# Performance work log

Hardware: AMD Instinct MI355X
Metric: run time of the kernel (lower is better)

Reference implementation:

```python
import jax, jax.numpy as jnp
import numpy as np

N_NODES = 50000
N_EDGES = 800000
D = 64
NEG_SLOPE = 0.2


def setup_inputs() -> dict:
    key = jax.random.key(0)
    ks = jax.random.split(key, 16)
    inp = {
        "t": jnp.zeros((1,), jnp.float32),
        "x": jax.random.normal(ks[0], (N_NODES, D), jnp.float32),
        "edge_index": jax.random.randint(ks[1], (2, N_EDGES), 0, N_NODES, jnp.int64),
    }
    # 3 GATConv layers (64->64, 64->64, 64->64), heads=1
    s = 1.0 / np.sqrt(D)
    for li, k0 in zip((1, 2, 3), (2, 6, 10)):
        inp[f"W{li}"] = jax.random.normal(ks[k0], (D, D), jnp.float32) * s
        inp[f"a_src{li}"] = jax.random.normal(ks[k0 + 1], (D,), jnp.float32) * s
        inp[f"a_dst{li}"] = jax.random.normal(ks[k0 + 2], (D,), jnp.float32) * s
        inp[f"b{li}"] = jnp.zeros((D,), jnp.float32)
    return inp


def _gat_conv(x, src, dst, W, a_src, a_dst, b):
    # h = W x  (PyG: lin(x)), per-edge attention, segment softmax over dst
    n = x.shape[0]
    h = x @ W                                   # [N, D]
    score = jax.nn.leaky_relu(h[src] @ a_src + h[dst] @ a_dst, NEG_SLOPE)  # [E]
    smax = jax.ops.segment_max(score, dst, num_segments=n)                 # [N]
    ex = jnp.exp(score - smax[dst])                                        # [E]
    denom = jax.ops.segment_sum(ex, dst, num_segments=n)                   # [N]
    alpha = ex / denom[dst]                                                # [E]
    out = jax.ops.segment_sum(alpha[:, None] * h[src], dst, num_segments=n)
    return out + b


def reference(t, x, edge_index, W1, a_src1, a_dst1, b1, W2, a_src2, a_dst2, b2, W3, a_src3, a_dst3, b3):
    n = x.shape[0]
    # PyG GATConv default add_self_loops=True
    loops = jnp.arange(n, dtype=edge_index.dtype)
    src = jnp.concatenate([edge_index[0], loops])
    dst = jnp.concatenate([edge_index[1], loops])
    h = _gat_conv(x, src, dst, W1, a_src1, a_dst1, b1)
    h = jax.nn.relu(h)
    h = _gat_conv(h, src, dst, W2, a_src2, a_dst2, b2)
    h = jax.nn.relu(h)
    h = _gat_conv(h, src, dst, W3, a_src3, a_dst3, b3)
    return h
```

## Files before the change

### kernel.cpp

```cpp
#include <hip/hip_runtime.h>
#include <hip/hip_fp16.h>

#define NN 50000
#define NE 800000
#define D 64
#define GB ((NN + 63) / 64)
#define NBUCK ((NN + 127) >> 7)
#define CHUNK 4096
#define EBLKS ((NE + CHUNK - 1) / CHUNK)
#define CAPB 4096

__device__ __forceinline__ float lrelu(float s) { return (s > 0.0f) ? s : 0.2f * s; }


__device__ __forceinline__ void bin_pass_body(int blk, const int* __restrict__ ei,
                                              int* __restrict__ gcur,
                                              unsigned* __restrict__ pairs,
                                              int* cnt_loc, int* base_loc) {
  int t = threadIdx.x;
  int e0 = blk * CHUNK;
  int n = (NE - e0 < CHUNK) ? (NE - e0) : CHUNK;
  for (int i = t; i < NBUCK; i += 256) cnt_loc[i] = 0;
  __syncthreads();
  for (int i = t; i < n; i += 256)
    atomicAdd(&cnt_loc[ei[NE + e0 + i] >> 7], 1);
  __syncthreads();
  for (int i = t; i < NBUCK; i += 256) {
    int c = cnt_loc[i];
    base_loc[i] = c ? (i * CAPB + atomicAdd(&gcur[i], c)) : 0;
    cnt_loc[i] = 0;
  }
  __syncthreads();
  for (int i = t; i < n; i += 256) {
    int src = ei[e0 + i];
    int dst = ei[NE + e0 + i];
    int b = dst >> 7;
    int off = atomicAdd(&cnt_loc[b], 1);
    unsigned pk = ((unsigned)src << 7) | (unsigned)(dst & 127);
    __builtin_nontemporal_store(pk, &pairs[base_loc[b] + off]);
  }
}

__device__ __forceinline__ void gemm_body(int gblk, const float* __restrict__ xin,
                                          const float* __restrict__ W,
                                          const float* __restrict__ a_src,
                                          const float* __restrict__ a_dst,
                                          __half* __restrict__ h16,
                                          float* __restrict__ s_src,
                                          float* __restrict__ s_dst, int do_relu,
                                          float* wlds, float (*xT)[68],
                                          float (*psrc)[17], float (*pdst)[17]) {
  int t = threadIdx.x;
  int n0 = gblk * 64;

  const float4* W4 = (const float4*)W;
  float4* wl4 = (float4*)wlds;
#pragma unroll
  for (int i = 0; i < 4; ++i) wl4[t + 256 * i] = W4[t + 256 * i];

#pragma unroll
  for (int i = 0; i < 4; ++i) {
    int idx = t + 256 * i;
    int r = idx >> 4, c4 = idx & 15;
    int n = n0 + r;
    float4 v = make_float4(0.f, 0.f, 0.f, 0.f);
    if (n < NN) v = ((const float4*)xin)[(size_t)n * 16 + c4];
    if (do_relu) {
      v.x = fmaxf(v.x, 0.f); v.y = fmaxf(v.y, 0.f);
      v.z = fmaxf(v.z, 0.f); v.w = fmaxf(v.w, 0.f);
    }
    xT[c4 * 4 + 0][r] = v.x;
    xT[c4 * 4 + 1][r] = v.y;
    xT[c4 * 4 + 2][r] = v.z;
    xT[c4 * 4 + 3][r] = v.w;
  }
  __syncthreads();

  int tr = t & 15, tc = t >> 4;
  float acc[4][4] = {};
#pragma unroll 8
  for (int k = 0; k < 64; ++k) {
    float4 xa = *(const float4*)&xT[k][tr * 4];
    float4 wv = *(const float4*)&wlds[k * 64 + tc * 4];
    float xs[4] = {xa.x, xa.y, xa.z, xa.w};
    float wj[4] = {wv.x, wv.y, wv.z, wv.w};
#pragma unroll
    for (int i = 0; i < 4; ++i)
#pragma unroll
      for (int j = 0; j < 4; ++j) acc[i][j] = fmaf(xs[i], wj[j], acc[i][j]);
  }

#pragma unroll
  for (int i = 0; i < 4; ++i) {
    int n = n0 + tr * 4 + i;
    if (n < NN) {
      __half2* dst = (__half2*)&h16[(size_t)n * 64 + tc * 4];
      dst[0] = __floats2half2_rn(acc[i][0], acc[i][1]);
      dst[1] = __floats2half2_rn(acc[i][2], acc[i][3]);
    }
  }

  float as[4], ad[4];
#pragma unroll
  for (int j = 0; j < 4; ++j) { as[j] = a_src[tc * 4 + j]; ad[j] = a_dst[tc * 4 + j]; }
#pragma unroll
  for (int i = 0; i < 4; ++i) {
    float p1 = 0.f, p2 = 0.f;
#pragma unroll
    for (int j = 0; j < 4; ++j) { p1 = fmaf(acc[i][j], as[j], p1); p2 = fmaf(acc[i][j], ad[j], p2); }
    psrc[tr * 4 + i][tc] = p1;
    pdst[tr * 4 + i][tc] = p2;
  }
  __syncthreads();
  if (t < 64) {
    int n = n0 + t;
    if (n < NN) {
      float s1 = 0.f, s2 = 0.f;
#pragma unroll
      for (int c = 0; c < 16; ++c) { s1 += psrc[t][c]; s2 += pdst[t][c]; }
      s_src[n] = s1;
      s_dst[n] = s2;
    }
  }
}


__global__ __launch_bounds__(256) void bin_gemm1(
    const int* __restrict__ ei, int* __restrict__ gcur, unsigned* __restrict__ pairs,
    const float* __restrict__ xin, const float* __restrict__ W,
    const float* __restrict__ a_src, const float* __restrict__ a_dst,
    __half* __restrict__ h16, float* __restrict__ s_src, float* __restrict__ s_dst) {
  __shared__ float wlds[64 * 64];
  __shared__ float xT[64][68];
  __shared__ float psrc[64][17];
  __shared__ float pdst[64][17];
  __shared__ int cnt_loc[NBUCK];
  __shared__ int base_loc[NBUCK];
  if (blockIdx.x < EBLKS) {
    bin_pass_body(blockIdx.x, ei, gcur, pairs, cnt_loc, base_loc);
  } else {
    gemm_body(blockIdx.x - EBLKS, xin, W, a_src, a_dst, h16, s_src, s_dst, 0,
              wlds, xT, psrc, pdst);
  }
}

__global__ __launch_bounds__(256) void gemm_feat(
    const float* __restrict__ xin, const float* __restrict__ W,
    const float* __restrict__ a_src, const float* __restrict__ a_dst,
    __half* __restrict__ h16, float* __restrict__ s_src, float* __restrict__ s_dst,
    int do_relu) {
  __shared__ float wlds[64 * 64];
  __shared__ float xT[64][68];
  __shared__ float psrc[64][17];
  __shared__ float pdst[64][17];
  gemm_body(blockIdx.x, xin, W, a_src, a_dst, h16, s_src, s_dst, do_relu,
            wlds, xT, psrc, pdst);
}

__global__ __launch_bounds__(256) void bucket_sort(const unsigned* __restrict__ pairs,
                                                   const int* __restrict__ gcur,
                                                   int* __restrict__ row_start,
                                                   int* __restrict__ deg,
                                                   int* __restrict__ sorted_src) {
  __shared__ int cnt[128];
  __shared__ int exc[128];
  __shared__ int cur[128];
  __shared__ int buf[CAPB];
  int b = blockIdx.x;
  int t = threadIdx.x;
  int n0 = b << 7;
  int start = b * CAPB;
  int cntb = gcur[b];
  if (cntb > CAPB) cntb = CAPB;
  if (t < 128) cnt[t] = 0;
  __syncthreads();
  for (int i = t; i < cntb; i += 256)
    atomicAdd(&cnt[pairs[start + i] & 127u], 1);
  __syncthreads();
  if (t < 128) exc[t] = cnt[t];
  __syncthreads();
  for (int s = 1; s < 128; s <<= 1) {
    int add = 0;
    if (t < 128 && t >= s) add = exc[t - s];
    __syncthreads();
    if (t < 128) exc[t] += add;
    __syncthreads();
  }
  if (t < 128) {
    int e = exc[t] - cnt[t];
    cur[t] = e;
    int nd = n0 + t;
    if (nd < NN) {
      row_start[nd] = start + e;
      deg[nd] = cnt[t];
    }
  }
  __syncthreads();
  for (int i = t; i < cntb; i += 256) {
    unsigned pk = pairs[start + i];
    int pos = atomicAdd(&cur[pk & 127u], 1);
    if (pos < CAPB) buf[pos] = (int)(pk >> 7);
  }
  __syncthreads();
  for (int i = t; i < cntb; i += 256)
    sorted_src[start + i] = buf[i];
}

__global__ void agg_kernel(const int* __restrict__ sorted_src, const int* __restrict__ row_start,
                           const int* __restrict__ deg, const float* __restrict__ s_src,
                           const float* __restrict__ s_dst, const __half* __restrict__ h16,
                           const float* __restrict__ bias, float* __restrict__ out) {
  int gid = blockIdx.x * blockDim.x + threadIdx.x;
  int n = gid >> 5;
  if (n >= NN) return;
  int lane = threadIdx.x & 31;
  int start = row_start[n];
  int dg = deg[n];
  float sdn = s_dst[n];
  float sself = lrelu(s_src[n] + sdn);
  float exself = __expf(sself - 8.0f);

  float2 acc;
  {
    float2 f = __half22float2(*(const __half2*)&h16[(size_t)n * 64 + 2 * lane]);
    acc.x = exself * f.x;
    acc.y = exself * f.y;
  }
  float dpart = 0.0f;
  for (int base = 0; base < dg; base += 32) {
    int i = base + lane;
    bool act = (i < dg);
    int msrc = act ? __builtin_nontemporal_load(&sorted_src[start + i]) : 0;
    float s = act ? lrelu(s_src[msrc] + sdn) : -INFINITY;
    float ex = __expf(s - 8.0f);
    dpart += ex;
    unsigned pk = ((unsigned)msrc << 16) |
                  (unsigned)__half_as_ushort(__float2half_rn(ex));
    int nch = (dg - base < 32) ? (dg - base) : 32;
    for (int b0 = 0; b0 < nch; b0 += 8) {
      unsigned pu[8]; unsigned vv[8];
#pragma unroll
      for (int e = 0; e < 8; ++e)
        pu[e] = __shfl(pk, b0 + e, 32);
#pragma unroll
      for (int e = 0; e < 8; ++e)
        vv[e] = *(const unsigned*)&h16[(size_t)(pu[e] >> 16) * 64 + 2 * lane];
#pragma unroll
      for (int e = 0; e < 8; ++e) {
        float xf = __half2float(__ushort_as_half((unsigned short)(pu[e] & 0xFFFFu)));
        float2 f = __half22float2(*(__half2*)&vv[e]);
        acc.x = fmaf(xf, f.x, acc.x);
        acc.y = fmaf(xf, f.y, acc.y);
      }
    }
  }
#pragma unroll
  for (int off = 16; off > 0; off >>= 1)
    dpart += __shfl_xor(dpart, off, 32);
  float d = exself + dpart;
  float2 bv = *(const float2*)&bias[2 * lane];
  float2 o;
  o.x = acc.x / d + bv.x;
  o.y = acc.y / d + bv.y;
  *(float2*)&out[(size_t)n * 64 + 2 * lane] = o;
}


extern "C" void kernel_launch(void* const* d_in, const int* in_sizes, int n_in,
                              void* d_out, int out_size, void* d_ws, size_t ws_size,
                              hipStream_t stream) {
  const float* x  = (const float*)d_in[1];
  const int*   ei = (const int*)d_in[2];
  const float* W1 = (const float*)d_in[3];
  const float* as1 = (const float*)d_in[4];
  const float* ad1 = (const float*)d_in[5];
  const float* b1 = (const float*)d_in[6];
  const float* W2 = (const float*)d_in[7];
  const float* as2 = (const float*)d_in[8];
  const float* ad2 = (const float*)d_in[9];
  const float* b2 = (const float*)d_in[10];
  const float* W3 = (const float*)d_in[11];
  const float* as3 = (const float*)d_in[12];
  const float* ad3 = (const float*)d_in[13];
  const float* b3 = (const float*)d_in[14];
  float* out = (float*)d_out;

  const size_t ND = (size_t)NN * D;
  char* base = (char*)d_ws;
  __half* h16    = (__half*)base;
  float* A       = (float*)(base + ND * 2);
  float* B       = A + ND;
  float* s_src   = B + ND;
  float* s_dst   = s_src + NN;
  int* row_start = (int*)(s_dst + NN);
  int* deg       = row_start + NN;
  int* gcur      = deg + NN;
  int* sorted_src= gcur + NBUCK;
  unsigned* pairs = (unsigned*)A;

  const int AGG_BLOCKS = (NN * 32 + 255) / 256;

  hipMemsetAsync(gcur, 0, (size_t)NBUCK * sizeof(int), stream);
  bin_gemm1<<<EBLKS + GB, 256, 0, stream>>>(ei, gcur, pairs, x, W1, as1, ad1,
                                            h16, s_src, s_dst);
  bucket_sort<<<NBUCK, 256, 0, stream>>>(pairs, gcur, row_start, deg, sorted_src);

  agg_kernel<<<AGG_BLOCKS, 256, 0, stream>>>(sorted_src, row_start, deg, s_src, s_dst,
                                             h16, b1, A);
  gemm_feat<<<GB, 256, 0, stream>>>(A, W2, as2, ad2, h16, s_src, s_dst, 1);
  agg_kernel<<<AGG_BLOCKS, 256, 0, stream>>>(sorted_src, row_start, deg, s_src, s_dst,
                                             h16, b2, B);
  gemm_feat<<<GB, 256, 0, stream>>>(B, W3, as3, ad3, h16, s_src, s_dst, 1);
  agg_kernel<<<AGG_BLOCKS, 256, 0, stream>>>(sorted_src, row_start, deg, s_src, s_dst,
                                             h16, b3, out);
}
```

Measured before the change: 149.8 us.

## Pair layer-1 GEMM with bucket sort and widen aggregation gather unroll

The first-layer feature GEMM moves out of the edge-binning kernel and is co-launched with the bucket sort instead. The binning pass becomes its own small-LDS kernel. Shared memory for the sort and GEMM branches is overlaid in one byte arena. This lets the binning kernel run at higher occupancy, and hides the serial sort behind GEMM work. The aggregation kernel's neighbor gather is also unrolled from 8 to 16 loads per batch, giving more loads in flight at the cost of more registers.

Result: slower. 155.2 us (+3.6%).

```diff
diff --git a/kernel.cpp b/kernel.cpp
--- a/kernel.cpp
+++ b/kernel.cpp
@@ -9,16 +9,18 @@
 #define CHUNK 4096
 #define EBLKS ((NE + CHUNK - 1) / CHUNK)
 #define CAPB 4096
+#define ARENA_BYTES (16384 + 17408 + 4352 + 4352)
 
 __device__ __forceinline__ float lrelu(float s) { return (s > 0.0f) ? s : 0.2f * s; }
 
 
-__device__ __forceinline__ void bin_pass_body(int blk, const int* __restrict__ ei,
-                                              int* __restrict__ gcur,
-                                              unsigned* __restrict__ pairs,
-                                              int* cnt_loc, int* base_loc) {
+__global__ __launch_bounds__(256) void bin_pass(const int* __restrict__ ei,
+                                                int* __restrict__ gcur,
+                                                unsigned* __restrict__ pairs) {
+  __shared__ int cnt_loc[NBUCK];
+  __shared__ int base_loc[NBUCK];
   int t = threadIdx.x;
-  int e0 = blk * CHUNK;
+  int e0 = blockIdx.x * CHUNK;
   int n = (NE - e0 < CHUNK) ? (NE - e0) : CHUNK;
   for (int i = t; i < NBUCK; i += 256) cnt_loc[i] = 0;
   __syncthreads();
@@ -41,6 +43,54 @@
   }
 }
 
+__device__ __forceinline__ void sort_body(int b, const unsigned* __restrict__ pairs,
+                                          const int* __restrict__ gcur,
+                                          int* __restrict__ row_start,
+                                          int* __restrict__ deg,
+                                          int* __restrict__ sorted_src, char* arena) {
+  int* cnt = (int*)arena;
+  int* exc = cnt + 128;
+  int* cur = exc + 128;
+  int* buf = cur + 128;
+  int t = threadIdx.x;
+  int n0 = b << 7;
+  int start = b * CAPB;
+  int cntb = gcur[b];
+  if (cntb > CAPB) cntb = CAPB;
+  if (t < 128) cnt[t] = 0;
+  __syncthreads();
+  for (int i = t; i < cntb; i += 256)
+    atomicAdd(&cnt[pairs[start + i] & 127u], 1);
+  __syncthreads();
+  if (t < 128) exc[t] = cnt[t];
+  __syncthreads();
+  for (int s = 1; s < 128; s <<= 1) {
+    int add = 0;
+    if (t < 128 && t >= s) add = exc[t - s];
+    __syncthreads();
+    if (t < 128) exc[t] += add;
+    __syncthreads();
+  }
+  if (t < 128) {
+    int e = exc[t] - cnt[t];
+    cur[t] = e;
+    int nd = n0 + t;
+    if (nd < NN) {
+      row_start[nd] = start + e;
+      deg[nd] = cnt[t];
+    }
+  }
+  __syncthreads();
+  for (int i = t; i < cntb; i += 256) {
+    unsigned pk = pairs[start + i];
+    int pos = atomicAdd(&cur[pk & 127u], 1);
+    if (pos < CAPB) buf[pos] = (int)(pk >> 7);
+  }
+  __syncthreads();
+  for (int i = t; i < cntb; i += 256)
+    sorted_src[start + i] = buf[i];
+}
+
 __device__ __forceinline__ void gemm_body(int gblk, const float* __restrict__ xin,
                                           const float* __restrict__ W,
                                           const float* __restrict__ a_src,
@@ -48,8 +98,11 @@
                                           __half* __restrict__ h16,
                                           float* __restrict__ s_src,
                                           float* __restrict__ s_dst, int do_relu,
-                                          float* wlds, float (*xT)[68],
-                                          float (*psrc)[17], float (*pdst)[17]) {
+                                          char* arena) {
+  float* wlds = (float*)arena;
+  float (*xT)[68] = (float (*)[68])(arena + 16384);
+  float (*psrc)[17] = (float (*)[17])(arena + 16384 + 17408);
+  float (*pdst)[17] = (float (*)[17])(arena + 16384 + 17408 + 4352);
   int t = threadIdx.x;
   int n0 = gblk * 64;
 
@@ -125,22 +178,17 @@
 }
 
 
-__global__ __launch_bounds__(256) void bin_gemm1(
-    const int* __restrict__ ei, int* __restrict__ gcur, unsigned* __restrict__ pairs,
+__global__ __launch_bounds__(256) void sort_gemm1(
+    const unsigned* __restrict__ pairs, const int* __restrict__ gcur,
+    int* __restrict__ row_start, int* __restrict__ deg, int* __restrict__ sorted_src,
     const float* __restrict__ xin, const float* __restrict__ W,
     const float* __restrict__ a_src, const float* __restrict__ a_dst,
     __half* __restrict__ h16, float* __restrict__ s_src, float* __restrict__ s_dst) {
-  __shared__ float wlds[64 * 64];
-  __shared__ float xT[64][68];
-  __shared__ float psrc[64][17];
-  __shared__ float pdst[64][17];
-  __shared__ int cnt_loc[NBUCK];
-  __shared__ int base_loc[NBUCK];
-  if (blockIdx.x < EBLKS) {
-    bin_pass_body(blockIdx.x, ei, gcur, pairs, cnt_loc, base_loc);
+  __shared__ __align__(16) char arena[ARENA_BYTES];
+  if (blockIdx.x < NBUCK) {
+    sort_body(blockIdx.x, pairs, gcur, row_start, deg, sorted_src, arena);
   } else {
-    gemm_body(blockIdx.x - EBLKS, xin, W, a_src, a_dst, h16, s_src, s_dst, 0,
-              wlds, xT, psrc, pdst);
+    gemm_body(blockIdx.x - NBUCK, xin, W, a_src, a_dst, h16, s_src, s_dst, 0, arena);
   }
 }
 
@@ -149,61 +197,8 @@
     const float* __restrict__ a_src, const float* __restrict__ a_dst,
     __half* __restrict__ h16, float* __restrict__ s_src, float* __restrict__ s_dst,
     int do_relu) {
-  __shared__ float wlds[64 * 64];
-  __shared__ float xT[64][68];
-  __shared__ float psrc[64][17];
-  __shared__ float pdst[64][17];
-  gemm_body(blockIdx.x, xin, W, a_src, a_dst, h16, s_src, s_dst, do_relu,
-            wlds, xT, psrc, pdst);
-}
-
-__global__ __launch_bounds__(256) void bucket_sort(const unsigned* __restrict__ pairs,
-                                                   const int* __restrict__ gcur,
-                                                   int* __restrict__ row_start,
-                                                   int* __restrict__ deg,
-                                                   int* __restrict__ sorted_src) {
-  __shared__ int cnt[128];
-  __shared__ int exc[128];
-  __shared__ int cur[128];
-  __shared__ int buf[CAPB];
-  int b = blockIdx.x;
-  int t = threadIdx.x;
-  int n0 = b << 7;
-  int start = b * CAPB;
-  int cntb = gcur[b];
-  if (cntb > CAPB) cntb = CAPB;
-  if (t < 128) cnt[t] = 0;
-  __syncthreads();
-  for (int i = t; i < cntb; i += 256)
-    atomicAdd(&cnt[pairs[start + i] & 127u], 1);
-  __syncthreads();
-  if (t < 128) exc[t] = cnt[t];
-  __syncthreads();
-  for (int s = 1; s < 128; s <<= 1) {
-    int add = 0;
-    if (t < 128 && t >= s) add = exc[t - s];
-    __syncthreads();
-    if (t < 128) exc[t] += add;
-    __syncthreads();
-  }
-  if (t < 128) {
-    int e = exc[t] - cnt[t];
-    cur[t] = e;
-    int nd = n0 + t;
-    if (nd < NN) {
-      row_start[nd] = start + e;
-      deg[nd] = cnt[t];
-    }
-  }
-  __syncthreads();
-  for (int i = t; i < cntb; i += 256) {
-    unsigned pk = pairs[start + i];
-    int pos = atomicAdd(&cur[pk & 127u], 1);
-    if (pos < CAPB) buf[pos] = (int)(pk >> 7);
-  }
-  __syncthreads();
-  for (int i = t; i < cntb; i += 256)
-    sorted_src[start + i] = buf[i];
+  __shared__ __align__(16) char arena[ARENA_BYTES];
+  gemm_body(blockIdx.x, xin, W, a_src, a_dst, h16, s_src, s_dst, do_relu, arena);
 }
 
 __global__ void agg_kernel(const int* __restrict__ sorted_src, const int* __restrict__ row_start,
@@ -237,16 +232,16 @@
     unsigned pk = ((unsigned)msrc << 16) |
                   (unsigned)__half_as_ushort(__float2half_rn(ex));
     int nch = (dg - base < 32) ? (dg - base) : 32;
-    for (int b0 = 0; b0 < nch; b0 += 8) {
-      unsigned pu[8]; unsigned vv[8];
-#pragma unroll
-      for (int e = 0; e < 8; ++e)
+    for (int b0 = 0; b0 < nch; b0 += 16) {
+      unsigned pu[16]; unsigned vv[16];
+#pragma unroll
+      for (int e = 0; e < 16; ++e)
         pu[e] = __shfl(pk, b0 + e, 32);
 #pragma unroll
-      for (int e = 0; e < 8; ++e)
+      for (int e = 0; e < 16; ++e)
         vv[e] = *(const unsigned*)&h16[(size_t)(pu[e] >> 16) * 64 + 2 * lane];
 #pragma unroll
-      for (int e = 0; e < 8; ++e) {
+      for (int e = 0; e < 16; ++e) {
         float xf = __half2float(__ushort_as_half((unsigned short)(pu[e] & 0xFFFFu)));
         float2 f = __half22float2(*(__half2*)&vv[e]);
         acc.x = fmaf(xf, f.x, acc.x);
@@ -301,9 +296,9 @@
   const int AGG_BLOCKS = (NN * 32 + 255) / 256;
 
   hipMemsetAsync(gcur, 0, (size_t)NBUCK * sizeof(int), stream);
-  bin_gemm1<<<EBLKS + GB, 256, 0, stream>>>(ei, gcur, pairs, x, W1, as1, ad1,
-                                            h16, s_src, s_dst);
-  bucket_sort<<<NBUCK, 256, 0, stream>>>(pairs, gcur, row_start, deg, sorted_src);
+  bin_pass<<<EBLKS, 256, 0, stream>>>(ei, gcur, pairs);
+  sort_gemm1<<<NBUCK + GB, 256, 0, stream>>>(pairs, gcur, row_start, deg, sorted_src,
+                                             x, W1, as1, ad1, h16, s_src, s_dst);
 
   agg_kernel<<<AGG_BLOCKS, 256, 0, stream>>>(sorted_src, row_start, deg, s_src, s_dst,
                                              h16, b1, A);
```
